# Performance work log

Measured on AMD Instinct MI355X. Metric: run time of the kernel, lower is better.

The kernel has to match this reference:

```python
import jax, jax.numpy as jnp
import numpy as np

RADIUS = 3
TEMP = 0.1
EPS = 1e-6


def bilinear_resize(x, oh, ow):
    # Matches torch F.interpolate(mode='bilinear', align_corners=False):
    # half-pixel centers, source coord clamped to >= 0, no antialiasing.
    b, c, h, w = x.shape
    ys = jnp.maximum((jnp.arange(oh, dtype=x.dtype) + 0.5) * (h / oh) - 0.5, 0.0)
    xs = jnp.maximum((jnp.arange(ow, dtype=x.dtype) + 0.5) * (w / ow) - 0.5, 0.0)
    y0f = jnp.floor(ys)
    x0f = jnp.floor(xs)
    wy = (ys - y0f)[:, None]          # [oh,1]
    wx = (xs - x0f)[None, :]          # [1,ow]
    y0 = jnp.clip(y0f, 0, h - 1).astype(jnp.int32)
    y1 = jnp.clip(y0f + 1, 0, h - 1).astype(jnp.int32)
    x0 = jnp.clip(x0f, 0, w - 1).astype(jnp.int32)
    x1 = jnp.clip(x0f + 1, 0, w - 1).astype(jnp.int32)
    r0 = x[:, :, y0, :]
    r1 = x[:, :, y1, :]
    v00 = r0[:, :, :, x0]; v01 = r0[:, :, :, x1]
    v10 = r1[:, :, :, x0]; v11 = r1[:, :, :, x1]
    return (1 - wy) * ((1 - wx) * v00 + wx * v01) + wy * ((1 - wx) * v10 + wx * v11)


def setup_inputs() -> dict:
    key = jax.random.key(0)
    k1, k2, k3 = jax.random.split(key, 3)
    fL = jax.random.normal(k1, (4, 256, 96, 320), dtype=jnp.float32)
    fR = jax.random.normal(k2, (4, 256, 96, 320), dtype=jnp.float32)
    disp_full = jax.random.uniform(k3, (4, 1, 384, 1280), dtype=jnp.float32) * 64.0
    return {"fL": fL, "fR": fR, "disp_full": disp_full}


def reference(fL, fR, disp_full):
    B, C, h4, w4 = fL.shape
    H, W = disp_full.shape[-2], disp_full.shape[-1]
    # quarter-res disparity
    disp0 = bilinear_resize(disp_full, h4, w4) / 4.0            # [B,1,h4,w4]
    # cosine correlation volume over 2*radius+1 horizontal shifts
    nL = fL / jnp.clip(jnp.linalg.norm(fL, axis=1, keepdims=True), EPS)
    nR = fR / jnp.clip(jnp.linalg.norm(fR, axis=1, keepdims=True), EPS)
    sims = [jnp.sum(nL * jnp.roll(nR, d, axis=-1), axis=1)
            for d in range(-RADIUS, RADIUS + 1)]
    # original wraps build_cosine_cost in @torch.no_grad()
    cost = jax.lax.stop_gradient(jnp.stack(sims, axis=1))       # [B,7,h4,w4]
    p = jax.nn.softmax(cost / TEMP, axis=1)
    offsets = jnp.arange(-RADIUS, RADIUS + 1, dtype=fL.dtype).reshape(1, -1, 1, 1)
    delta = jnp.sum(p * offsets, axis=1, keepdims=True)          # [B,1,h4,w4]
    disp_ref = disp0 + delta
    conf = jnp.max(p, axis=1, keepdims=True)
    # laplacian smoothing (smooth=True)
    lap = jnp.array([[0., 1., 0.], [1., -4., 1.], [0., 1., 0.]], dtype=fL.dtype).reshape(1, 1, 3, 3)
    lap_out = jax.lax.conv_general_dilated(disp_ref, lap, (1, 1), [(1, 1), (1, 1)])
    disp_q = disp_ref - 0.2 * lap_out
    disp_full_ref = bilinear_resize(disp_q, H, W) * 4.0
    conf_full = bilinear_resize(conf, H, W)
    return disp_full_ref, conf_full
```

## Files before the change

### kernel.cpp

```cpp
#include <hip/hip_runtime.h>
#include <math.h>

constexpr int B_ = 4, C_ = 256, H4 = 96, W4 = 320, HF = 384, WF = 1280;
constexpr int CHUNKS = 5;
constexpr float EPSV = 1e-6f;
constexpr int LOW = B_ * H4 * W4;
constexpr int FULL = B_ * HF * WF;

__device__ __forceinline__ void accum_batch(
    const float4 vL, const float4 wA, const float4 wB, const float4 wC,
    const bool rsel, float* __restrict__ acc, float* __restrict__ sL,
    float* __restrict__ sR, float* __restrict__ sH)
{
    const float lv[4]  = {vL.x, vL.y, vL.z, vL.w};
    const float wv[12] = {wA.x, wA.y, wA.z, wA.w,
                          wB.x, wB.y, wB.z, wB.w,
                          wC.x, wC.y, wC.z, wC.w};
#pragma unroll
    for (int k = 0; k < 7; ++k)
#pragma unroll
        for (int p = 0; p < 4; ++p)
            acc[k * 4 + p] = fmaf(lv[p], wv[p + k + 1], acc[k * 4 + p]);
#pragma unroll
    for (int p = 0; p < 4; ++p) {
        sL[p] = fmaf(lv[p], lv[p], sL[p]);
        sR[p] = fmaf(wv[4 + p], wv[4 + p], sR[p]);
    }
#pragma unroll
    for (int j = 0; j < 3; ++j) {
        const float t = rsel ? wv[8 + j] : wv[1 + j];
        sH[j] = fmaf(t, t, sH[j]);
    }
}

__global__ __launch_bounds__(256)
void phase1(const float* __restrict__ fL, const float* __restrict__ fR,
            const float* __restrict__ D, float* __restrict__ dref,
            float* __restrict__ conf)
{
    const int bi = blockIdx.x;
    const int chunk = bi % CHUNKS;
    const int y = (bi / CHUNKS) % H4;
    const int b = bi / (CHUNKS * H4);
    const int tid = threadIdx.x;
    const int wave = tid >> 6;
    const int lane = tid & 63;
    const int q = lane & 15;
    const int csub = lane >> 4;
    const int x0 = chunk * 64;
    const int xo = x0 + 4 * q;

    const size_t chanStride = (size_t)H4 * W4;
    const size_t rowBase = (((size_t)b * C_) * H4 + y) * W4;

    int lx = xo - 4; if (lx < 0)   lx += W4;
    int rx = xo + 4; if (rx >= W4) rx -= W4;

    const int c0 = wave * 64 + csub;
    const float* pL = fL + rowBase + (size_t)c0 * chanStride;
    const float* pR = fR + rowBase + (size_t)c0 * chanStride;
    const size_t step = 4 * chanStride;

    float acc[28];
#pragma unroll
    for (int i = 0; i < 28; ++i) acc[i] = 0.f;
    float sL[4] = {0.f, 0.f, 0.f, 0.f};
    float sR[4] = {0.f, 0.f, 0.f, 0.f};
    float sH[3] = {0.f, 0.f, 0.f};
    const bool rsel = (q == 15);

    float4 vL = *(const float4*)(pL + xo);
    float4 wA = *(const float4*)(pR + lx);
    float4 wB = *(const float4*)(pR + xo);
    float4 wC = *(const float4*)(pR + rx);

    size_t off = 0;
    for (int it = 0; it < 16; ++it) {
        const float4 cL = vL, cA = wA, cB = wB, cC = wC;
        if (it < 15) {
            off += step;
            vL = *(const float4*)(pL + off + xo);
            wA = *(const float4*)(pR + off + lx);
            wB = *(const float4*)(pR + off + xo);
            wC = *(const float4*)(pR + off + rx);
        }
        accum_batch(cL, cA, cB, cC, rsel, acc, sL, sR, sH);
    }

#pragma unroll
    for (int i = 0; i < 28; ++i) {
        acc[i] += __shfl_xor(acc[i], 16);
        acc[i] += __shfl_xor(acc[i], 32);
    }
#pragma unroll
    for (int p = 0; p < 4; ++p) {
        sL[p] += __shfl_xor(sL[p], 16); sL[p] += __shfl_xor(sL[p], 32);
        sR[p] += __shfl_xor(sR[p], 16); sR[p] += __shfl_xor(sR[p], 32);
    }
#pragma unroll
    for (int j = 0; j < 3; ++j) {
        sH[j] += __shfl_xor(sH[j], 16);
        sH[j] += __shfl_xor(sH[j], 32);
    }

    __shared__ float rec[4][16][37];
    __shared__ float hrec[4][2][3];
    __shared__ float sss[70];
    if (lane < 16) {
#pragma unroll
        for (int i = 0; i < 28; ++i) rec[wave][lane][i] = acc[i];
#pragma unroll
        for (int p = 0; p < 4; ++p) {
            rec[wave][lane][28 + p] = sL[p];
            rec[wave][lane][32 + p] = sR[p];
        }
    }
    if (lane == 0) {
#pragma unroll
        for (int j = 0; j < 3; ++j) hrec[wave][0][j] = sH[j];
    }
    if (lane == 15) {
#pragma unroll
        for (int j = 0; j < 3; ++j) hrec[wave][1][j] = sH[j];
    }
    __syncthreads();

    float D7[7];
    float rsL = 0.f;
    if (tid < 64) {
        const int qq = tid >> 2, pp = tid & 3;
#pragma unroll
        for (int k = 0; k < 7; ++k)
            D7[k] = rec[0][qq][4 * k + pp] + rec[1][qq][4 * k + pp]
                  + rec[2][qq][4 * k + pp] + rec[3][qq][4 * k + pp];
        rsL = rec[0][qq][28 + pp] + rec[1][qq][28 + pp]
            + rec[2][qq][28 + pp] + rec[3][qq][28 + pp];
        const float rsR = rec[0][qq][32 + pp] + rec[1][qq][32 + pp]
                        + rec[2][qq][32 + pp] + rec[3][qq][32 + pp];
        sss[3 + tid] = rsR;
        if (tid < 3)
            sss[tid] = hrec[0][0][tid] + hrec[1][0][tid]
                     + hrec[2][0][tid] + hrec[3][0][tid];
        if (tid >= 61) {
            const int j = tid - 61;
            sss[67 + j] = hrec[0][1][j] + hrec[1][1][j]
                        + hrec[2][1][j] + hrec[3][1][j];
        }
    }
    __syncthreads();

    if (tid < 64) {
        const float nLv = fmaxf(sqrtf(rsL), EPSV);
        float cost[7];
#pragma unroll
        for (int k = 0; k < 7; ++k) {
            const float nR = fmaxf(sqrtf(sss[tid + k]), EPSV);
            cost[6 - k] = (D7[k] / (nLv * nR)) * 10.0f;
        }
        float m = cost[0];
#pragma unroll
        for (int i = 1; i < 7; ++i) m = fmaxf(m, cost[i]);
        float sum = 0.f, dsum = 0.f;
#pragma unroll
        for (int i = 0; i < 7; ++i) {
            const float e = __expf(cost[i] - m);
            sum += e;
            dsum += e * (float)(i - 3);
        }
        const float delta = dsum / sum;
        const float cf = 1.0f / sum;

        const int xpix = x0 + tid;
        const int Y0 = 4 * y + 1, X0 = 4 * xpix + 1;
        const size_t dbase = ((size_t)b * HF + Y0) * WF + X0;
        const float s4 = D[dbase] + D[dbase + 1] + D[dbase + WF] + D[dbase + WF + 1];
        const float disp0 = s4 * 0.0625f;

        const size_t o = ((size_t)b * H4 + y) * W4 + xpix;
        dref[o] = disp0 + delta;
        conf[o] = cf;
    }
}

__device__ __forceinline__ float dq_val(const float* __restrict__ dref,
                                        size_t base, int yq, int xq)
{
    size_t i = base + (size_t)yq * W4 + xq;
    float c  = dref[i];
    float up = (yq > 0)      ? dref[i - W4] : 0.f;
    float dn = (yq < H4 - 1) ? dref[i + W4] : 0.f;
    float lf = (xq > 0)      ? dref[i - 1]  : 0.f;
    float rt = (xq < W4 - 1) ? dref[i + 1]  : 0.f;
    return c - 0.2f * (up + dn + lf + rt - 4.f * c);
}

__global__ void phase2(const float* __restrict__ dref, const float* __restrict__ cf,
                       float* __restrict__ out)
{
    int i = blockIdx.x * blockDim.x + threadIdx.x;
    if (i >= FULL) return;
    int X = i % WF;
    int Y = (i / WF) % HF;
    int b = i / (WF * HF);
    float ys = fmaxf((Y + 0.5f) * 0.25f - 0.5f, 0.f);
    float xs = fmaxf((X + 0.5f) * 0.25f - 0.5f, 0.f);
    float y0f = floorf(ys), x0f = floorf(xs);
    float wy = ys - y0f, wx = xs - x0f;
    int y0 = min((int)y0f, H4 - 1);
    int x0 = min((int)x0f, W4 - 1);
    int y1 = min(y0 + 1, H4 - 1);
    int x1 = min(x0 + 1, W4 - 1);
    size_t base = (size_t)b * (H4 * W4);

    float d = (1.f - wy) * ((1.f - wx) * dq_val(dref, base, y0, x0) + wx * dq_val(dref, base, y0, x1))
            +        wy  * ((1.f - wx) * dq_val(dref, base, y1, x0) + wx * dq_val(dref, base, y1, x1));

    size_t i00 = base + (size_t)y0 * W4 + x0;
    size_t i01 = base + (size_t)y0 * W4 + x1;
    size_t i10 = base + (size_t)y1 * W4 + x0;
    size_t i11 = base + (size_t)y1 * W4 + x1;
    float cv = (1.f - wy) * ((1.f - wx) * cf[i00] + wx * cf[i01])
             +        wy  * ((1.f - wx) * cf[i10] + wx * cf[i11]);

    out[i] = 4.0f * d;
    out[(size_t)FULL + i] = cv;
}

extern "C" void kernel_launch(void* const* d_in, const int* in_sizes, int n_in,
                              void* d_out, int out_size, void* d_ws, size_t ws_size,
                              hipStream_t stream)
{
    const float* fL = (const float*)d_in[0];
    const float* fR = (const float*)d_in[1];
    const float* D  = (const float*)d_in[2];
    float* out  = (float*)d_out;
    float* ws   = (float*)d_ws;
    float* dref = ws;
    float* conf = ws + LOW;

    phase1<<<B_ * H4 * CHUNKS, 256, 0, stream>>>(fL, fR, D, dref, conf);
    phase2<<<(FULL + 255) / 256, 256, 0, stream>>>(dref, conf, out);
}
```

Before: 287.0 us.

## Deepen phase1 load prefetch to two stages and vectorize phase2 upsampling per 4 pixels

Phase1 now keeps a three-slot register ring so loads run two channel groups ahead of the FMA work, with the loop fully unrolled and compiler barriers added. The aim is to hide more global-memory latency. Phase2 now has each thread produce four horizontally adjacent full-resolution pixels. It uses the fixed 4x bilinear weights, computes three vertically-interpolated columns once and writes float4 stores, which cuts redundant smoothed-disparity evaluations and index math. The costs are higher register pressure in phase1 and hardcoded interpolation weights that only hold for the exact 4x scale.

```diff
diff --git a/kernel.cpp b/kernel.cpp
--- a/kernel.cpp
+++ b/kernel.cpp
@@ -69,22 +69,31 @@
     float sH[3] = {0.f, 0.f, 0.f};
     const bool rsel = (q == 15);
 
-    float4 vL = *(const float4*)(pL + xo);
-    float4 wA = *(const float4*)(pR + lx);
-    float4 wB = *(const float4*)(pR + xo);
-    float4 wC = *(const float4*)(pR + rx);
-
-    size_t off = 0;
+    float4 bL[3], bA[3], bB[3], bC[3];
+
+#pragma unroll
+    for (int g = 0; g < 2; ++g) {
+        const size_t o = (size_t)g * step;
+        bL[g] = *(const float4*)(pL + o + xo);
+        bA[g] = *(const float4*)(pR + o + lx);
+        bB[g] = *(const float4*)(pR + o + xo);
+        bC[g] = *(const float4*)(pR + o + rx);
+    }
+    asm volatile("" ::: "memory");
+
+#pragma unroll
     for (int it = 0; it < 16; ++it) {
-        const float4 cL = vL, cA = wA, cB = wB, cC = wC;
-        if (it < 15) {
-            off += step;
-            vL = *(const float4*)(pL + off + xo);
-            wA = *(const float4*)(pR + off + lx);
-            wB = *(const float4*)(pR + off + xo);
-            wC = *(const float4*)(pR + off + rx);
-        }
-        accum_batch(cL, cA, cB, cC, rsel, acc, sL, sR, sH);
+        const int cur = it % 3;
+        if (it + 2 < 16) {
+            const int nxt = (it + 2) % 3;
+            const size_t o = (size_t)(it + 2) * step;
+            bL[nxt] = *(const float4*)(pL + o + xo);
+            bA[nxt] = *(const float4*)(pR + o + lx);
+            bB[nxt] = *(const float4*)(pR + o + xo);
+            bC[nxt] = *(const float4*)(pR + o + rx);
+        }
+        asm volatile("" ::: "memory");
+        accum_batch(bL[cur], bA[cur], bB[cur], bC[cur], rsel, acc, sL, sR, sH);
     }
 
 #pragma unroll
@@ -197,33 +206,47 @@
 __global__ void phase2(const float* __restrict__ dref, const float* __restrict__ cf,
                        float* __restrict__ out)
 {
-    int i = blockIdx.x * blockDim.x + threadIdx.x;
-    if (i >= FULL) return;
-    int X = i % WF;
-    int Y = (i / WF) % HF;
-    int b = i / (WF * HF);
-    float ys = fmaxf((Y + 0.5f) * 0.25f - 0.5f, 0.f);
-    float xs = fmaxf((X + 0.5f) * 0.25f - 0.5f, 0.f);
-    float y0f = floorf(ys), x0f = floorf(xs);
-    float wy = ys - y0f, wx = xs - x0f;
-    int y0 = min((int)y0f, H4 - 1);
-    int x0 = min((int)x0f, W4 - 1);
-    int y1 = min(y0 + 1, H4 - 1);
-    int x1 = min(x0 + 1, W4 - 1);
-    size_t base = (size_t)b * (H4 * W4);
-
-    float d = (1.f - wy) * ((1.f - wx) * dq_val(dref, base, y0, x0) + wx * dq_val(dref, base, y0, x1))
-            +        wy  * ((1.f - wx) * dq_val(dref, base, y1, x0) + wx * dq_val(dref, base, y1, x1));
-
-    size_t i00 = base + (size_t)y0 * W4 + x0;
-    size_t i01 = base + (size_t)y0 * W4 + x1;
-    size_t i10 = base + (size_t)y1 * W4 + x0;
-    size_t i11 = base + (size_t)y1 * W4 + x1;
-    float cv = (1.f - wy) * ((1.f - wx) * cf[i00] + wx * cf[i01])
-             +        wy  * ((1.f - wx) * cf[i10] + wx * cf[i11]);
-
-    out[i] = 4.0f * d;
-    out[(size_t)FULL + i] = cv;
+    const int idx = blockIdx.x * blockDim.x + threadIdx.x;
+    constexpr int WQ = WF / 4;
+    if (idx >= FULL / 4) return;
+    const int k = idx % WQ;
+    const int Y = (idx / WQ) % HF;
+    const int b = idx / (WQ * HF);
+
+    const float ys = fmaxf((Y + 0.5f) * 0.25f - 0.5f, 0.f);
+    const float y0f = floorf(ys);
+    const float wy = ys - y0f;
+    const int y0 = min((int)y0f, H4 - 1);
+    const int y1 = min(y0 + 1, H4 - 1);
+    const size_t base = (size_t)b * (H4 * W4);
+
+    const int xa = max(k - 1, 0);
+    const int xb = k;
+    const int xc = min(k + 1, W4 - 1);
+
+    const float da = (1.f - wy) * dq_val(dref, base, y0, xa) + wy * dq_val(dref, base, y1, xa);
+    const float db = (1.f - wy) * dq_val(dref, base, y0, xb) + wy * dq_val(dref, base, y1, xb);
+    const float dc = (1.f - wy) * dq_val(dref, base, y0, xc) + wy * dq_val(dref, base, y1, xc);
+
+    const size_t r0 = base + (size_t)y0 * W4;
+    const size_t r1 = base + (size_t)y1 * W4;
+    const float ca = (1.f - wy) * cf[r0 + xa] + wy * cf[r1 + xa];
+    const float cb = (1.f - wy) * cf[r0 + xb] + wy * cf[r1 + xb];
+    const float cc = (1.f - wy) * cf[r0 + xc] + wy * cf[r1 + xc];
+
+    float4 dv, cv;
+    dv.x = 4.0f * (0.375f * da + 0.625f * db);
+    dv.y = 4.0f * (0.125f * da + 0.875f * db);
+    dv.z = 4.0f * (0.875f * db + 0.125f * dc);
+    dv.w = 4.0f * (0.625f * db + 0.375f * dc);
+    cv.x = 0.375f * ca + 0.625f * cb;
+    cv.y = 0.125f * ca + 0.875f * cb;
+    cv.z = 0.875f * cb + 0.125f * cc;
+    cv.w = 0.625f * cb + 0.375f * cc;
+
+    const size_t o = (((size_t)b * HF + Y) * WF) + 4 * k;
+    *(float4*)&out[o] = dv;
+    *(float4*)&out[(size_t)FULL + o] = cv;
 }
 
 extern "C" void kernel_launch(void* const* d_in, const int* in_sizes, int n_in,
@@ -239,5 +262,5 @@
     float* conf = ws + LOW;
 
     phase1<<<B_ * H4 * CHUNKS, 256, 0, stream>>>(fL, fR, D, dref, conf);
-    phase2<<<(FULL + 255) / 256, 256, 0, stream>>>(dref, conf, out);
-}
+    phase2<<<(FULL / 4 + 255) / 256, 256, 0, stream>>>(dref, conf, out);
+}
```

After: 282.6 us. Within noise of the previous version (-1.5%).
